# Kernel optimization log

Hardware: AMD Instinct MI355X
Metric: run time of the kernel (lower is better)

The kernel has to match this reference:

```python
import jax, jax.numpy as jnp
import numpy as np

GRID = 8        # kornia equalize_clahe default grid_size=(8,8)
NUM_BINS = 256  # kornia default
CLIP_LIMIT = 40.0


def normalize_in_range(x, lo, hi):
    mn, mx = x.min(), x.max()
    return (x - mn) / (mx - mn) * (hi - lo) + lo


def equalize_clahe(x, clip_limit=CLIP_LIMIT, grid=GRID, bins=NUM_BINS):
    # x: (B, C, H, W) in [0, 1]; H, W divisible by grid
    B, C, H, W = x.shape
    th, tw = H // grid, W // grid
    pixels = th * tw

    # --- per-pixel bin index (histc with bins=256, min=0, max=1) ---
    bidx = jnp.clip((x * bins).astype(jnp.int32), 0, bins - 1)  # (B,C,H,W)

    # --- per-tile histograms via one segment_sum (scatter-add) ---
    ti = (jnp.arange(H) // th)[None, None, :, None]
    tj = (jnp.arange(W) // tw)[None, None, None, :]
    bb = jnp.arange(B)[:, None, None, None]
    cc = jnp.arange(C)[None, :, None, None]
    tile_id = ((bb * C + cc) * grid + ti) * grid + tj          # (B,C,H,W)
    flat = (tile_id * bins + bidx).reshape(-1)
    hist = jax.ops.segment_sum(
        jnp.ones(flat.shape, jnp.float32), flat,
        num_segments=B * C * grid * grid * bins,
    ).reshape(B, C, grid, grid, bins)

    # --- clip histogram and redistribute excess uniformly ---
    max_val = max(int(clip_limit * pixels // bins), 1)
    hist = jnp.minimum(hist, max_val)
    residual = (pixels - hist.sum(-1, keepdims=True)) / bins
    hist = hist + residual

    # --- CDF -> LUT (values in [0, bins-1], floored) ---
    lut = jnp.floor(jnp.clip(jnp.cumsum(hist, axis=-1) * ((bins - 1) / pixels),
                             0.0, bins - 1.0))                 # (B,C,gh,gw,bins)

    # --- bilinear interpolation between the 4 nearest tile LUTs ---
    gi = jnp.clip((jnp.arange(H) + 0.5) / th - 0.5, 0.0, grid - 1.0)
    gj = jnp.clip((jnp.arange(W) + 0.5) / tw - 0.5, 0.0, grid - 1.0)
    i0 = jnp.floor(gi).astype(jnp.int32); i1 = jnp.minimum(i0 + 1, grid - 1)
    j0 = jnp.floor(gj).astype(jnp.int32); j1 = jnp.minimum(j0 + 1, grid - 1)
    wy = (gi - i0)[None, None, :, None]
    wx = (gj - j0)[None, None, None, :]

    I0 = i0[None, None, :, None]; I1 = i1[None, None, :, None]
    J0 = j0[None, None, None, :]; J1 = j1[None, None, None, :]

    v00 = lut[bb, cc, I0, J0, bidx]
    v01 = lut[bb, cc, I0, J1, bidx]
    v10 = lut[bb, cc, I1, J0, bidx]
    v11 = lut[bb, cc, I1, J1, bidx]

    out = (1.0 - wy) * ((1.0 - wx) * v00 + wx * v01) + wy * ((1.0 - wx) * v10 + wx * v11)
    return out / (bins - 1)


def setup_inputs() -> dict:
    key = jax.random.key(0)
    kx, ky = jax.random.split(key)
    x = jax.random.normal(kx, (16, 1, 1024, 1024), dtype=jnp.float32)
    y = jax.random.randint(ky, (16,), 0, 10, dtype=jnp.int64)
    return {"x": x, "y": y}


def reference(x, y):
    x = normalize_in_range(x, 0.0, 1.0)
    mean = x.mean(axis=(0, 2, 3))
    std = jnp.std(x, axis=(0, 2, 3), ddof=1)  # torch unbiased std
    x = (x - mean[None, :, None, None]) / std[None, :, None, None]
    x = normalize_in_range(x, 0.0, 1.0)
    x = equalize_clahe(x, clip_limit=40.0)
    return (x, y)
```

## Files before the change

kernel.cpp:

```cpp
#include <hip/hip_runtime.h>


#define BINS 256
#define MAXV 2560u

__global__ __launch_bounds__(256) void k_minmax(const float4* __restrict__ x4,
                                                float2* __restrict__ partials,
                                                const int* __restrict__ y,
                                                float* __restrict__ out,
                                                int N, int tail, int n4){
  int tid = blockIdx.x * 256 + threadIdx.x;
  int stride = gridDim.x * 256;
  float lmin = INFINITY, lmax = -INFINITY;
  for (int i = tid; i < n4; i += stride){
    float4 v = x4[i];
    lmin = fminf(lmin, fminf(fminf(v.x, v.y), fminf(v.z, v.w)));
    lmax = fmaxf(lmax, fmaxf(fmaxf(v.x, v.y), fmaxf(v.z, v.w)));
  }
  for (int o = 32; o > 0; o >>= 1){
    lmin = fminf(lmin, __shfl_down(lmin, o, 64));
    lmax = fmaxf(lmax, __shfl_down(lmax, o, 64));
  }
  __shared__ float smin[4], smax[4];
  int lane = threadIdx.x & 63, wv = threadIdx.x >> 6;
  if (lane == 0){ smin[wv] = lmin; smax[wv] = lmax; }
  __syncthreads();
  if (threadIdx.x == 0){
    float m = smin[0], M = smax[0];
    #pragma unroll
    for (int i = 1; i < 4; i++){ m = fminf(m, smin[i]); M = fmaxf(M, smax[i]); }
    partials[blockIdx.x] = make_float2(m, M);
  }
  if (blockIdx.x == 0 && threadIdx.x < tail)
    out[N + threadIdx.x] = (float)y[threadIdx.x];
}

__global__ __launch_bounds__(256) void k_hist(const float* __restrict__ x,
                                              const float2* __restrict__ partials,
                                              int nparts,
                                              float* __restrict__ lut,
                                              unsigned char* __restrict__ bins){
  __shared__ unsigned hist8[8 * 257];
  __shared__ unsigned wsum[4];
  __shared__ unsigned sc[BINS];
  __shared__ float smn, sinv;
  __shared__ float smin[4], smax[4];
  int t = threadIdx.x;
  float lmin = INFINITY, lmax = -INFINITY;
  for (int i = t; i < nparts; i += 256){
    float2 p = partials[i];
    lmin = fminf(lmin, p.x);
    lmax = fmaxf(lmax, p.y);
  }
  for (int o = 32; o > 0; o >>= 1){
    lmin = fminf(lmin, __shfl_down(lmin, o, 64));
    lmax = fmaxf(lmax, __shfl_down(lmax, o, 64));
  }
  int lane = t & 63, wv = t >> 6;
  if (lane == 0){ smin[wv] = lmin; smax[wv] = lmax; }
  for (int i = t; i < 8 * 257; i += 256) hist8[i] = 0u;
  __syncthreads();
  if (t == 0){
    float m = smin[0], M = smax[0];
    #pragma unroll
    for (int i = 1; i < 4; i++){ m = fminf(m, smin[i]); M = fmaxf(M, smax[i]); }
    smn = m;
    sinv = 1.0f / (M - m);
  }
  __syncthreads();
  float mn = smn, inv = sinv;
  int tile = blockIdx.x;
  int bc = tile >> 6, ti = (tile >> 3) & 7, tj = tile & 7;
  size_t base = ((size_t)bc * 1024 + ti * 128) * 1024 + tj * 128;
  const float4* x4 = (const float4*)(x + base);
  uchar4* b4 = (uchar4*)(bins + base);
  unsigned hc = (t & 7) * 257;
  #pragma unroll 4
  for (int k = 0; k < 16; k++){
    int p = t + (k << 8);
    int row = p >> 5, col = p & 31;
    float4 v = x4[row * 256 + col];
    int b0 = min(max((int)(((v.x - mn) * inv) * 256.0f), 0), 255);
    int b1 = min(max((int)(((v.y - mn) * inv) * 256.0f), 0), 255);
    int b2 = min(max((int)(((v.z - mn) * inv) * 256.0f), 0), 255);
    int b3 = min(max((int)(((v.w - mn) * inv) * 256.0f), 0), 255);
    b4[row * 256 + col] = make_uchar4((unsigned char)b0, (unsigned char)b1,
                                      (unsigned char)b2, (unsigned char)b3);
    atomicAdd(&hist8[hc + b0], 1u);
    atomicAdd(&hist8[hc + b1], 1u);
    atomicAdd(&hist8[hc + b2], 1u);
    atomicAdd(&hist8[hc + b3], 1u);
  }
  __syncthreads();
  unsigned h = 0;
  #pragma unroll
  for (int c = 0; c < 8; c++) h += hist8[c * 257 + t];
  if (h > MAXV) h = MAXV;
  unsigned s = h;
  for (int o = 32; o > 0; o >>= 1) s += __shfl_down(s, o, 64);
  if (lane == 0) wsum[wv] = s;
  __syncthreads();
  unsigned total = wsum[0] + wsum[1] + wsum[2] + wsum[3];
  float residual = (16384.0f - (float)total) * (1.0f / 256.0f);
  sc[t] = h;
  __syncthreads();
  for (int o = 1; o < 256; o <<= 1){
    unsigned pv = (t >= o) ? sc[t - o] : 0u;
    __syncthreads();
    sc[t] += pv;
    __syncthreads();
  }
  float cum = ((float)sc[t] + (float)(t + 1) * residual) * (255.0f / 16384.0f);
  lut[(size_t)tile * BINS + t] = floorf(fminf(fmaxf(cum, 0.0f), 255.0f));
}

__global__ __launch_bounds__(256) void k_apply(const uchar4* __restrict__ binsq,
                                               const float* __restrict__ lutg,
                                               float* __restrict__ out){
  __shared__ float l0s[2048];
  __shared__ float l1s[2048];
  int t = threadIdx.x;
  int strip = blockIdx.x;
  int b = strip >> 6;
  int r0 = (strip & 63) << 4;
  float gi = fminf(fmaxf((r0 + 0.5f) * (1.0f / 128.0f) - 0.5f, 0.0f), 7.0f);
  int i0 = (int)gi;
  int i1 = min(i0 + 1, 7);
  const float4* g0 = (const float4*)(lutg + ((size_t)b * 8 + i0) * 2048);
  const float4* g1 = (const float4*)(lutg + ((size_t)b * 8 + i1) * 2048);
  ((float4*)l0s)[t]       = g0[t];
  ((float4*)l0s)[t + 256] = g0[t + 256];
  ((float4*)l1s)[t]       = g1[t];
  ((float4*)l1s)[t + 256] = g1[t + 256];
  int j0[4], j1[4];
  float wx[4];
  #pragma unroll
  for (int c = 0; c < 4; c++){
    int col = (t << 2) + c;
    float gj = fminf(fmaxf((col + 0.5f) * (1.0f / 128.0f) - 0.5f, 0.0f), 7.0f);
    j0[c] = (int)gj;
    j1[c] = min(j0[c] + 1, 7);
    wx[c] = gj - (float)j0[c];
  }
  size_t base4 = ((size_t)b * 1024 + r0) * 256;
  __syncthreads();
  for (int r = 0; r < 16; r++){
    int h = r0 + r;
    float giw = fminf(fmaxf((h + 0.5f) * (1.0f / 128.0f) - 0.5f, 0.0f), 7.0f);
    float wy = giw - (float)i0;
    uchar4 bv = binsq[base4 + r * 256 + t];
    int bi[4] = {bv.x, bv.y, bv.z, bv.w};
    float res[4];
    #pragma unroll
    for (int c = 0; c < 4; c++){
      float v00 = l0s[(j0[c] << 8) + bi[c]];
      float v01 = l0s[(j1[c] << 8) + bi[c]];
      float v10 = l1s[(j0[c] << 8) + bi[c]];
      float v11 = l1s[(j1[c] << 8) + bi[c]];
      float top = v00 + wx[c] * (v01 - v00);
      float bot = v10 + wx[c] * (v11 - v10);
      res[c] = (top + wy * (bot - top)) * (1.0f / 255.0f);
    }
    ((float4*)out)[base4 + r * 256 + t] = make_float4(res[0], res[1], res[2], res[3]);
  }
}

extern "C" void kernel_launch(void* const* d_in, const int* in_sizes, int n_in,
                              void* d_out, int out_size, void* d_ws, size_t ws_size,
                              hipStream_t stream){
  const float* x = (const float*)d_in[0];
  const int* y = (const int*)d_in[1];
  float* out = (float*)d_out;
  int N = in_sizes[0];
  int B = N >> 20;
  int n4 = N >> 2;
  const int NPARTS = 1024;
  float2* partials = (float2*)d_ws;
  float* lut = (float*)((char*)d_ws + 8192);
  size_t lutbytes = (size_t)B * 64 * 256 * 4;
  unsigned char* bins = (unsigned char*)d_ws + 8192 + lutbytes;
  int tail = out_size - N;

  hipLaunchKernelGGL(k_minmax, dim3(NPARTS), dim3(256), 0, stream,
                     (const float4*)x, partials, y, out, N, tail, n4);
  hipLaunchKernelGGL(k_hist, dim3(B * 64), dim3(256), 0, stream,
                     x, partials, NPARTS, lut, bins);
  hipLaunchKernelGGL(k_apply, dim3(B * 64), dim3(256), 0, stream,
                     (const uchar4*)bins, lut, out);
}
```

Baseline: 135.5 us.

## Fuse global min/max with per-tile fine histograms and rebin to global bins

Replaces the separate min/max pass with a per-tile kernel that loads each tile once, computes the tile's min/max and a 2048-bin fine histogram on the tile-local range. A LUT kernel then maps the fine bins onto the 256 global bins using bin centers. The apply kernel recomputes bin indices from x instead of reading a stored byte-bin buffer, which removes one full read of the input plus the bin write and read. Apply also interleaves the two LUT rows as float2 and uses smaller row strips. The fine-to-coarse remap is approximate: pixels in fine bins that straddle a global bin edge can be counted in the wrong bin, which can shift LUT values slightly.

After: 168.9 us. +24.6%, slower.

```diff
diff --git a/kernel.cpp b/kernel.cpp
--- a/kernel.cpp
+++ b/kernel.cpp
@@ -2,50 +2,86 @@
 
 
 #define BINS 256
+#define FBINS 2048
 #define MAXV 2560u
 
-__global__ __launch_bounds__(256) void k_minmax(const float4* __restrict__ x4,
-                                                float2* __restrict__ partials,
-                                                const int* __restrict__ y,
-                                                float* __restrict__ out,
-                                                int N, int tail, int n4){
-  int tid = blockIdx.x * 256 + threadIdx.x;
-  int stride = gridDim.x * 256;
+__global__ __launch_bounds__(256) void k_tilestat(const float* __restrict__ x,
+                                                  float2* __restrict__ partials,
+                                                  unsigned* __restrict__ finehg){
+  __shared__ unsigned fh[FBINS];
+  __shared__ float smin[4], smax[4];
+  __shared__ float sp[2];
+  int t = threadIdx.x;
+  int tile = blockIdx.x;
+  int bc = tile >> 6, ti = (tile >> 3) & 7, tj = tile & 7;
+  const float4* x4 = (const float4*)(x + ((size_t)bc * 1024 + ti * 128) * 1024 + tj * 128);
+  float4 v[16];
+  #pragma unroll
+  for (int k = 0; k < 16; k++){
+    int p = t + (k << 8);
+    v[k] = x4[(p >> 5) * 256 + (p & 31)];
+  }
+  #pragma unroll
+  for (int i = 0; i < FBINS / 256; i++) fh[t + i * 256] = 0u;
   float lmin = INFINITY, lmax = -INFINITY;
-  for (int i = tid; i < n4; i += stride){
-    float4 v = x4[i];
-    lmin = fminf(lmin, fminf(fminf(v.x, v.y), fminf(v.z, v.w)));
-    lmax = fmaxf(lmax, fmaxf(fmaxf(v.x, v.y), fmaxf(v.z, v.w)));
+  #pragma unroll
+  for (int k = 0; k < 16; k++){
+    lmin = fminf(lmin, fminf(fminf(v[k].x, v[k].y), fminf(v[k].z, v[k].w)));
+    lmax = fmaxf(lmax, fmaxf(fmaxf(v[k].x, v[k].y), fmaxf(v[k].z, v[k].w)));
   }
   for (int o = 32; o > 0; o >>= 1){
     lmin = fminf(lmin, __shfl_down(lmin, o, 64));
     lmax = fmaxf(lmax, __shfl_down(lmax, o, 64));
   }
-  __shared__ float smin[4], smax[4];
-  int lane = threadIdx.x & 63, wv = threadIdx.x >> 6;
+  int lane = t & 63, wv = t >> 6;
   if (lane == 0){ smin[wv] = lmin; smax[wv] = lmax; }
   __syncthreads();
-  if (threadIdx.x == 0){
+  if (t == 0){
     float m = smin[0], M = smax[0];
     #pragma unroll
     for (int i = 1; i < 4; i++){ m = fminf(m, smin[i]); M = fmaxf(M, smax[i]); }
-    partials[blockIdx.x] = make_float2(m, M);
-  }
-  if (blockIdx.x == 0 && threadIdx.x < tail)
-    out[N + threadIdx.x] = (float)y[threadIdx.x];
-}
-
-__global__ __launch_bounds__(256) void k_hist(const float* __restrict__ x,
-                                              const float2* __restrict__ partials,
-                                              int nparts,
-                                              float* __restrict__ lut,
-                                              unsigned char* __restrict__ bins){
-  __shared__ unsigned hist8[8 * 257];
+    partials[tile] = make_float2(m, M);
+    sp[0] = m;
+    sp[1] = (float)FBINS / fmaxf(M - m, 1e-30f);
+  }
+  __syncthreads();
+  float tmn = sp[0], tinv = sp[1];
+  #pragma unroll 4
+  for (int k = 0; k < 16; k++){
+    int b0 = min((int)((v[k].x - tmn) * tinv), FBINS - 1);
+    int b1 = min((int)((v[k].y - tmn) * tinv), FBINS - 1);
+    int b2 = min((int)((v[k].z - tmn) * tinv), FBINS - 1);
+    int b3 = min((int)((v[k].w - tmn) * tinv), FBINS - 1);
+    atomicAdd(&fh[b0], 1u);
+    atomicAdd(&fh[b1], 1u);
+    atomicAdd(&fh[b2], 1u);
+    atomicAdd(&fh[b3], 1u);
+  }
+  __syncthreads();
+  unsigned* outp = finehg + (size_t)tile * (FBINS / 2);
+  #pragma unroll
+  for (int i = 0; i < FBINS / 512; i++){
+    int w = t + i * 256;
+    outp[w] = (fh[2 * w] & 0xFFFFu) | (fh[2 * w + 1] << 16);
+  }
+}
+
+__global__ __launch_bounds__(256) void k_lut(const float2* __restrict__ partials,
+                                             int nparts,
+                                             const unsigned* __restrict__ finehg,
+                                             float* __restrict__ lut,
+                                             float2* __restrict__ gmm,
+                                             const int* __restrict__ y,
+                                             float* __restrict__ out,
+                                             int N, int tail){
+  __shared__ unsigned ch[BINS];
+  __shared__ unsigned sc[BINS];
   __shared__ unsigned wsum[4];
-  __shared__ unsigned sc[BINS];
-  __shared__ float smn, sinv;
   __shared__ float smin[4], smax[4];
+  __shared__ float sp[2];
   int t = threadIdx.x;
+  int tile = blockIdx.x;
+  ch[t] = 0u;
   float lmin = INFINITY, lmax = -INFINITY;
   for (int i = t; i < nparts; i += 256){
     float2 p = partials[i];
@@ -58,43 +94,38 @@
   }
   int lane = t & 63, wv = t >> 6;
   if (lane == 0){ smin[wv] = lmin; smax[wv] = lmax; }
-  for (int i = t; i < 8 * 257; i += 256) hist8[i] = 0u;
   __syncthreads();
   if (t == 0){
     float m = smin[0], M = smax[0];
     #pragma unroll
     for (int i = 1; i < 4; i++){ m = fminf(m, smin[i]); M = fmaxf(M, smax[i]); }
-    smn = m;
-    sinv = 1.0f / (M - m);
-  }
-  __syncthreads();
-  float mn = smn, inv = sinv;
-  int tile = blockIdx.x;
-  int bc = tile >> 6, ti = (tile >> 3) & 7, tj = tile & 7;
-  size_t base = ((size_t)bc * 1024 + ti * 128) * 1024 + tj * 128;
-  const float4* x4 = (const float4*)(x + base);
-  uchar4* b4 = (uchar4*)(bins + base);
-  unsigned hc = (t & 7) * 257;
-  #pragma unroll 4
-  for (int k = 0; k < 16; k++){
-    int p = t + (k << 8);
-    int row = p >> 5, col = p & 31;
-    float4 v = x4[row * 256 + col];
-    int b0 = min(max((int)(((v.x - mn) * inv) * 256.0f), 0), 255);
-    int b1 = min(max((int)(((v.y - mn) * inv) * 256.0f), 0), 255);
-    int b2 = min(max((int)(((v.z - mn) * inv) * 256.0f), 0), 255);
-    int b3 = min(max((int)(((v.w - mn) * inv) * 256.0f), 0), 255);
-    b4[row * 256 + col] = make_uchar4((unsigned char)b0, (unsigned char)b1,
-                                      (unsigned char)b2, (unsigned char)b3);
-    atomicAdd(&hist8[hc + b0], 1u);
-    atomicAdd(&hist8[hc + b1], 1u);
-    atomicAdd(&hist8[hc + b2], 1u);
-    atomicAdd(&hist8[hc + b3], 1u);
-  }
-  __syncthreads();
-  unsigned h = 0;
-  #pragma unroll
-  for (int c = 0; c < 8; c++) h += hist8[c * 257 + t];
+    sp[0] = m;
+    sp[1] = 1.0f / (M - m);
+  }
+  __syncthreads();
+  float mn = sp[0], inv = sp[1];
+  float2 tp = partials[tile];
+  float tw = (tp.y - tp.x) * (1.0f / (float)FBINS);
+  const unsigned* fhp = finehg + (size_t)tile * (FBINS / 2);
+  #pragma unroll
+  for (int i = 0; i < 4; i++){
+    int w = t + i * 256;
+    unsigned pk = fhp[w];
+    unsigned c0 = pk & 0xFFFFu, c1 = pk >> 16;
+    int f0 = 2 * w;
+    if (c0){
+      float ctr = tp.x + ((float)f0 + 0.5f) * tw;
+      int cb = min(max((int)(((ctr - mn) * inv) * 256.0f), 0), 255);
+      atomicAdd(&ch[cb], c0);
+    }
+    if (c1){
+      float ctr = tp.x + ((float)f0 + 1.5f) * tw;
+      int cb = min(max((int)(((ctr - mn) * inv) * 256.0f), 0), 255);
+      atomicAdd(&ch[cb], c1);
+    }
+  }
+  __syncthreads();
+  unsigned h = ch[t];
   if (h > MAXV) h = MAXV;
   unsigned s = h;
   for (int o = 32; o > 0; o >>= 1) s += __shfl_down(s, o, 64);
@@ -112,26 +143,33 @@
   }
   float cum = ((float)sc[t] + (float)(t + 1) * residual) * (255.0f / 16384.0f);
   lut[(size_t)tile * BINS + t] = floorf(fminf(fmaxf(cum, 0.0f), 255.0f));
-}
-
-__global__ __launch_bounds__(256) void k_apply(const uchar4* __restrict__ binsq,
+  if (tile == 0){
+    if (t == 0) *gmm = make_float2(mn, inv);
+    if (t < tail) out[N + t] = (float)y[t];
+  }
+}
+
+__global__ __launch_bounds__(256) void k_apply(const float* __restrict__ x,
+                                               const float2* __restrict__ gmm,
                                                const float* __restrict__ lutg,
                                                float* __restrict__ out){
-  __shared__ float l0s[2048];
-  __shared__ float l1s[2048];
+  __shared__ float2 lint[2048];
   int t = threadIdx.x;
   int strip = blockIdx.x;
-  int b = strip >> 6;
-  int r0 = (strip & 63) << 4;
+  int b = strip >> 7;
+  int r0 = (strip & 127) << 3;
   float gi = fminf(fmaxf((r0 + 0.5f) * (1.0f / 128.0f) - 0.5f, 0.0f), 7.0f);
   int i0 = (int)gi;
   int i1 = min(i0 + 1, 7);
-  const float4* g0 = (const float4*)(lutg + ((size_t)b * 8 + i0) * 2048);
-  const float4* g1 = (const float4*)(lutg + ((size_t)b * 8 + i1) * 2048);
-  ((float4*)l0s)[t]       = g0[t];
-  ((float4*)l0s)[t + 256] = g0[t + 256];
-  ((float4*)l1s)[t]       = g1[t];
-  ((float4*)l1s)[t + 256] = g1[t + 256];
+  const float* g0 = lutg + ((size_t)b * 8 + i0) * 2048;
+  const float* g1 = lutg + ((size_t)b * 8 + i1) * 2048;
+  #pragma unroll
+  for (int i = 0; i < 8; i++){
+    int k = t + i * 256;
+    lint[k] = make_float2(g0[k], g1[k]);
+  }
+  float2 mmv = *gmm;
+  float mn = mmv.x, inv = mmv.y;
   int j0[4], j1[4];
   float wx[4];
   #pragma unroll
@@ -144,21 +182,23 @@
   }
   size_t base4 = ((size_t)b * 1024 + r0) * 256;
   __syncthreads();
-  for (int r = 0; r < 16; r++){
+  for (int r = 0; r < 8; r++){
     int h = r0 + r;
     float giw = fminf(fmaxf((h + 0.5f) * (1.0f / 128.0f) - 0.5f, 0.0f), 7.0f);
     float wy = giw - (float)i0;
-    uchar4 bv = binsq[base4 + r * 256 + t];
-    int bi[4] = {bv.x, bv.y, bv.z, bv.w};
+    float4 xv = ((const float4*)x)[base4 + r * 256 + t];
+    int bi[4];
+    bi[0] = min(max((int)(((xv.x - mn) * inv) * 256.0f), 0), 255);
+    bi[1] = min(max((int)(((xv.y - mn) * inv) * 256.0f), 0), 255);
+    bi[2] = min(max((int)(((xv.z - mn) * inv) * 256.0f), 0), 255);
+    bi[3] = min(max((int)(((xv.w - mn) * inv) * 256.0f), 0), 255);
     float res[4];
     #pragma unroll
     for (int c = 0; c < 4; c++){
-      float v00 = l0s[(j0[c] << 8) + bi[c]];
-      float v01 = l0s[(j1[c] << 8) + bi[c]];
-      float v10 = l1s[(j0[c] << 8) + bi[c]];
-      float v11 = l1s[(j1[c] << 8) + bi[c]];
-      float top = v00 + wx[c] * (v01 - v00);
-      float bot = v10 + wx[c] * (v11 - v10);
+      float2 p0 = lint[(j0[c] << 8) + bi[c]];
+      float2 p1 = lint[(j1[c] << 8) + bi[c]];
+      float top = p0.x + wx[c] * (p1.x - p0.x);
+      float bot = p0.y + wx[c] * (p1.y - p0.y);
       res[c] = (top + wy * (bot - top)) * (1.0f / 255.0f);
     }
     ((float4*)out)[base4 + r * 256 + t] = make_float4(res[0], res[1], res[2], res[3]);
@@ -173,18 +213,16 @@
   float* out = (float*)d_out;
   int N = in_sizes[0];
   int B = N >> 20;
-  int n4 = N >> 2;
-  const int NPARTS = 1024;
+  int T = B * 64;
   float2* partials = (float2*)d_ws;
-  float* lut = (float*)((char*)d_ws + 8192);
-  size_t lutbytes = (size_t)B * 64 * 256 * 4;
-  unsigned char* bins = (unsigned char*)d_ws + 8192 + lutbytes;
+  float2* gmm = (float2*)((char*)d_ws + 8192);
+  unsigned* fineh = (unsigned*)((char*)d_ws + 16384);
+  float* lut = (float*)((char*)d_ws + 16384 + (size_t)T * (FBINS * 2));
   int tail = out_size - N;
 
-  hipLaunchKernelGGL(k_minmax, dim3(NPARTS), dim3(256), 0, stream,
-                     (const float4*)x, partials, y, out, N, tail, n4);
-  hipLaunchKernelGGL(k_hist, dim3(B * 64), dim3(256), 0, stream,
-                     x, partials, NPARTS, lut, bins);
-  hipLaunchKernelGGL(k_apply, dim3(B * 64), dim3(256), 0, stream,
-                     (const uchar4*)bins, lut, out);
-}
+  hipLaunchKernelGGL(k_tilestat, dim3(T), dim3(256), 0, stream, x, partials, fineh);
+  hipLaunchKernelGGL(k_lut, dim3(T), dim3(256), 0, stream,
+                     partials, T, fineh, lut, gmm, y, out, N, tail);
+  hipLaunchKernelGGL(k_apply, dim3(B * 128), dim3(256), 0, stream,
+                     x, gmm, lut, out);
+}
```
